# Kernel tuning notes

Measured on AMD Instinct MI355X. Metric: run time of the kernel, lower is better.

The kernel has to match this reference:

```python
import jax, jax.numpy as jnp
import numpy as np
import math

# Dims: d_model=192, expand=2 -> d_inner=d_ssm=384, headdim=64 -> nheads=6,
# d_state=128, K=4 scan directions, ngroups=1 (directions fused into state dim).
D_MODEL = 192
D_STATE = 128
D_CONV = 3
EXPAND = 2
HEADDIM = 64
CHUNK = 256
D_INNER = EXPAND * D_MODEL          # 384
D_SSM = D_INNER                     # default d_ssm (d_mlp == 0)
NHEADS = D_SSM // HEADDIM           # 6
K = 4                               # scan directions
HTOT = K * NHEADS                   # 24 heads in the fused scan
NSTATE = K * D_STATE                # 512 fused state dim (ngroups=1)
CONV_BC = 2 * D_STATE + NHEADS      # 262
B, H, W = 2, 64, 64


def _dwconv(x, w, b):
    # x: (B,C,H,W), w: (C,1,k,k) depthwise, SAME padding ((k-1)//2)
    y = jax.lax.conv_general_dilated(
        x, w, (1, 1), [(1, 1), (1, 1)],
        feature_group_count=x.shape[1],
        dimension_numbers=('NCHW', 'OIHW', 'NCHW'))
    return y + b[None, :, None, None]


def _ssd(x, dt_raw, A_logs, Bm, Cm, Ds, dt_bias):
    # Mamba2 chunked selective scan (dt_softplus=True, default dt_limit).
    # x: (b,l,h,p)  dt_raw: (b,l,h)  Bm,Cm: (b,l,n) with ngroups=1
    A = -jnp.exp(A_logs)                              # (h,)
    dt = jax.nn.softplus(dt_raw + dt_bias)            # (b,l,h)
    b, l, h, p = x.shape
    n = Bm.shape[-1]
    nc = l // CHUNK
    xc = x.reshape(b, nc, CHUNK, h, p)
    dtc = dt.reshape(b, nc, CHUNK, h)
    Bc = Bm.reshape(b, nc, CHUNK, n)
    Cc = Cm.reshape(b, nc, CHUNK, n)
    dA = dtc * A                                      # (b,nc,cs,h)
    acum = jnp.cumsum(dA, axis=2)
    # intra-chunk (causal, attention-like)
    a_t = jnp.transpose(acum, (0, 1, 3, 2))           # (b,nc,h,cs)
    diff = a_t[..., :, None] - a_t[..., None, :]      # (b,nc,h,i,j)
    causal = jnp.tril(jnp.ones((CHUNK, CHUNK), bool))
    Lmat = jnp.where(causal, jnp.exp(diff), 0.0)
    CB = jnp.einsum('bcin,bcjn->bcij', Cc, Bc)        # (b,nc,i,j)
    M = CB[:, :, None] * Lmat * jnp.transpose(dtc, (0, 1, 3, 2))[:, :, :, None, :]
    y = jnp.einsum('bchij,bcjhp->bcihp', M, xc)
    # chunk-final states
    decay_end = jnp.exp(acum[:, :, -1:, :] - acum)    # (b,nc,cs,h)
    states = jnp.einsum('bcjh,bcjn,bcjhp->bchpn', decay_end * dtc, Bc, xc)
    chunk_decay = jnp.exp(acum[:, :, -1, :])          # (b,nc,h)

    def step(S, inp):
        st, dec = inp
        return S * dec[:, :, None, None] + st, S

    S0 = jnp.zeros((b, h, p, n), x.dtype)
    _, prev = jax.lax.scan(step, S0, (jnp.moveaxis(states, 1, 0),
                                      jnp.moveaxis(chunk_decay, 1, 0)))
    prev = jnp.moveaxis(prev, 0, 1)                   # (b,nc,h,p,n)
    y = y + jnp.einsum('bcih,bcin,bchpn->bcihp', jnp.exp(acum), Cc, prev)
    y = y + xc * Ds[:, None]                          # D skip connection
    return y.reshape(b, l, h, p)


def _branch(u, u_cross, W_skip, W_xs, W_bcdt, conv_xs_w, conv_xs_b,
            conv_bc_w, conv_bc_b, dt_bias, A_logs, Ds, norm_w, W_out):
    Bb, Hh, Ww, _ = u.shape
    L = Hh * Ww
    z = (u @ W_skip).reshape(Bb, L, D_SSM)            # gate (d_mlp == 0)
    xs = jnp.transpose(u @ W_xs, (0, 3, 1, 2))        # (B,d_ssm,H,W)
    xs = jax.nn.silu(_dwconv(xs, conv_xs_w, conv_xs_b))
    bc = jnp.transpose(u_cross @ W_bcdt, (0, 3, 1, 2))
    bc = jax.nn.silu(_dwconv(bc, conv_bc_w, conv_bc_b))
    xbc = jnp.concatenate([xs, bc], axis=1)           # (B,646,H,W)
    C = xbc.shape[1]
    v = xbc.reshape(Bb, C, L)                         # HW raster
    vt = jnp.transpose(xbc, (0, 1, 3, 2)).reshape(Bb, C, L)  # WH raster
    hw = jnp.stack([v, vt], axis=1)                   # (B,2,C,L)
    xbcdt = jnp.concatenate([hw, jnp.flip(hw, axis=-1)], axis=1)  # (B,4,C,L)
    xp = xbcdt[:, :, :D_SSM]
    Bp = xbcdt[:, :, D_SSM:D_SSM + D_STATE]
    Cp = xbcdt[:, :, D_SSM + D_STATE:D_SSM + 2 * D_STATE]
    dtp = xbcdt[:, :, D_SSM + 2 * D_STATE:]
    x = xp.reshape(Bb, K * D_SSM, L).transpose(0, 2, 1).reshape(Bb, L, HTOT, HEADDIM)
    Bm = Bp.reshape(Bb, NSTATE, L).transpose(0, 2, 1)
    Cm = Cp.reshape(Bb, NSTATE, L).transpose(0, 2, 1)
    dt = dtp.reshape(Bb, HTOT, L).transpose(0, 2, 1)
    y = _ssd(x, dt, A_logs, Bm, Cm, Ds, dt_bias)      # (B,L,24,64)
    y = y.reshape(Bb, L, K, D_SSM)
    out_y = y[:, :, 0]
    inv_y = jnp.flip(y[:, :, 2:4], axis=1)            # (B,L,2,d_ssm)
    wh_y = y[:, :, 1].reshape(Bb, Ww, Hh, D_SSM).transpose(0, 2, 1, 3).reshape(Bb, L, D_SSM)
    invwh_y = inv_y[:, :, 1].reshape(Bb, Ww, Hh, D_SSM).transpose(0, 2, 1, 3).reshape(Bb, L, D_SSM)
    yf = out_y + inv_y[:, :, 0] + wh_y + invwh_y
    # gated RMSNorm (norm_before_gate=False, group_size == d_ssm)
    g = yf * jax.nn.silu(z)
    g = g * jax.lax.rsqrt(jnp.mean(g * g, axis=-1, keepdims=True) + 1e-5) * norm_w
    return (g @ W_out).reshape(Bb, Hh, Ww, D_MODEL)


def setup_inputs():
    key = jax.random.key(0)
    ks = jax.random.split(key, 16)
    f = lambda i, s: jax.random.normal(ks[i], s, jnp.float32)
    sc = 0.02
    dt = jnp.exp(jax.random.uniform(ks[10], (NHEADS,)) *
                 (math.log(0.1) - math.log(0.001)) + math.log(0.001))
    dt = jnp.maximum(dt, 1e-4)
    inv_dt = dt + jnp.log(-jnp.expm1(-dt))
    A = jax.random.uniform(ks[11], (NHEADS,), minval=1.0, maxval=16.0)
    return {
        'u1': f(0, (B, H, W, D_MODEL)),
        'u2': f(1, (B, H, W, D_MODEL)),
        'u2_cat_u1': f(2, (B, H, W, D_MODEL)),
        'u1_cat_u2': f(3, (B, H, W, D_MODEL)),
        'W_skip': f(4, (D_MODEL, D_SSM)) * sc,
        'W_xs': f(5, (D_MODEL, D_SSM)) * sc,
        'W_bcdt': f(6, (D_MODEL, CONV_BC)) * sc,
        'conv_xs_w': f(7, (D_SSM, 1, D_CONV, D_CONV)) * sc,
        'conv_xs_b': jnp.zeros((D_SSM,), jnp.float32),
        'conv_bc_w': f(8, (CONV_BC, 1, D_CONV, D_CONV)) * sc,
        'conv_bc_b': jnp.zeros((CONV_BC,), jnp.float32),
        'dt_bias': jnp.tile(inv_dt, K),
        'A_logs': jnp.tile(jnp.log(A), K),
        'Ds': jnp.ones((HTOT,), jnp.float32),
        'norm_w': jnp.ones((D_SSM,), jnp.float32),
        'W_out': f(9, (D_SSM, D_MODEL)) * sc,
    }


def reference(u1, u2, u2_cat_u1, u1_cat_u2, W_skip, W_xs, W_bcdt,
              conv_xs_w, conv_xs_b, conv_bc_w, conv_bc_b,
              dt_bias, A_logs, Ds, norm_w, W_out):
    args = (W_skip, W_xs, W_bcdt, conv_xs_w, conv_xs_b, conv_bc_w,
            conv_bc_b, dt_bias, A_logs, Ds, norm_w, W_out)
    out1 = _branch(u1, u2_cat_u1, *args)
    out2 = _branch(u2, u1_cat_u2, *args)
    return out1, out2
```

## Files before the change

### kernel.cpp

```cpp
#include <hip/hip_runtime.h>
#include <hip/hip_bf16.h>

#define DEV __device__ __forceinline__

static constexpr int LL   = 4096;
static constexpr int GG   = 4;
static constexpr int CBC  = 262;
static constexpr int BSTR = 264;

typedef float f32x4  __attribute__((ext_vector_type(4)));
typedef short bf16x8 __attribute__((ext_vector_type(8)));
typedef short bf16x4v __attribute__((ext_vector_type(4)));

DEV int map_l(int s, int k) {
    int m = (k & 2) ? (4095 - s) : s;
    if (k & 1) m = ((m & 63) << 6) | (m >> 6);
    return m;
}
DEV float silu_f(float x) { return x / (1.f + __expf(-x)); }
DEV short f2bf(float f) {
    union { __hip_bfloat16 h; short s; } u;
    u.h = __float2bfloat16(f);
    return u.s;
}
DEV float bf2f(short s) {
    return __uint_as_float(((unsigned)(unsigned short)s) << 16);
}
DEV bf16x8 pack8(float4 a, float4 b) {
    bf16x8 r;
    r[0]=f2bf(a.x); r[1]=f2bf(a.y); r[2]=f2bf(a.z); r[3]=f2bf(a.w);
    r[4]=f2bf(b.x); r[5]=f2bf(b.y); r[6]=f2bf(b.z); r[7]=f2bf(b.w);
    return r;
}
DEV bf16x8 load8u(const __hip_bfloat16* p) {
    bf16x4v lo = *(const bf16x4v*)p;
    bf16x4v hi = *(const bf16x4v*)(p + 4);
    bf16x8 r;
    r[0]=lo[0]; r[1]=lo[1]; r[2]=lo[2]; r[3]=lo[3];
    r[4]=hi[0]; r[5]=hi[1]; r[6]=hi[2]; r[7]=hi[3];
    return r;
}
DEV void store16(__hip_bfloat16* p, const float* v) {
    bf16x8 a, b;
    #pragma unroll
    for (int e = 0; e < 8; ++e) { a[e] = f2bf(v[e]); b[e] = f2bf(v[8+e]); }
    *(bf16x8*)p = a;
    *((bf16x8*)p + 1) = b;
}
DEV void storeT(float v, float* p) { *p = v; }
DEV void storeT(float v, __hip_bfloat16* p) { *p = __float2bfloat16(v); }

__global__ void sentinel_k(float* out) { out[0] = 1e30f; }

__global__ void wt_all_k(const float* __restrict__ W_skip, const float* __restrict__ W_xs,
                         const float* __restrict__ W_bcdt, const float* __restrict__ W_out,
                         __hip_bfloat16* __restrict__ Wt)
{
    int idx = blockIdx.x * 256 + threadIdx.x;
    if (idx < 73728) {
        int n = idx / 192, k = idx - n * 192;
        Wt[idx] = __float2bfloat16(W_skip[(size_t)k * 384 + n]);
    } else if (idx < 147456) {
        int r = idx - 73728;
        int n = r / 192, k = r - n * 192;
        Wt[idx] = __float2bfloat16(W_xs[(size_t)k * 384 + n]);
    } else if (idx < 208896) {
        int r = idx - 147456;
        int n = r / 192, k = r - n * 192;
        Wt[idx] = __float2bfloat16(n < 262 ? W_bcdt[(size_t)k * 262 + n] : 0.f);
    } else if (idx < 282624) {
        int r = idx - 208896;
        int n = r / 384, k = r - n * 384;
        Wt[idx] = __float2bfloat16(W_out[(size_t)k * 192 + n]);
    }
}

template<int MODE, typename AT, typename OutT>
__global__ __launch_bounds__(256) void mgemm_k(
    const AT* __restrict__ A0, const AT* __restrict__ A1,
    const __hip_bfloat16* __restrict__ Wt, OutT* __restrict__ C,
    OutT* __restrict__ C2, int N, int Kd)
{
    int i0 = blockIdx.y * 128;
    int j0 = blockIdx.x * 64;
    int t = threadIdx.x;
    int w = t >> 6, lane = t & 63;
    int lr = lane & 15, kq = lane >> 4;
    const AT* arow[2];
    #pragma unroll
    for (int a = 0; a < 2; ++a) {
        int grow = i0 + w * 32 + a * 16 + lr;
        const AT* Ap = (grow < 8192) ? A0 : A1;
        arow[a] = Ap + (size_t)(grow & 8191) * Kd;
    }
    f32x4 acc[2][4] = {};
    for (int k0 = 0; k0 < Kd; k0 += 32) {
        int kb = k0 + kq * 8;
        bf16x8 af[2];
        #pragma unroll
        for (int a = 0; a < 2; ++a) {
            if constexpr (sizeof(AT) == 4)
                af[a] = pack8(*(const float4*)(arow[a] + kb), *(const float4*)(arow[a] + kb + 4));
            else
                af[a] = *(const bf16x8*)(arow[a] + kb);
        }
        #pragma unroll
        for (int b = 0; b < 4; ++b) {
            int n = j0 + b * 16 + lr;
            bf16x8 bfr = *(const bf16x8*)(Wt + (size_t)n * Kd + kb);
            #pragma unroll
            for (int a = 0; a < 2; ++a)
                acc[a][b] = __builtin_amdgcn_mfma_f32_16x16x32_bf16(af[a], bfr, acc[a][b], 0, 0, 0);
        }
    }
    #pragma unroll
    for (int a = 0; a < 2; ++a)
        #pragma unroll
        for (int b = 0; b < 4; ++b)
            #pragma unroll
            for (int r = 0; r < 4; ++r) {
                int row = i0 + w * 32 + a * 16 + kq * 4 + r;
                int col = j0 + b * 16 + lr;
                float v = acc[a][b][r];
                if constexpr (MODE == 0) {
                    if (col < N) storeT(v, &C[(size_t)row * N + col]);
                } else if constexpr (MODE == 1) {
                    if (col < N) storeT(silu_f(v), &C[(size_t)row * N + col]);
                } else {
                    if (col < 384) storeT(silu_f(v), &C[(size_t)row * 384 + col]);
                    else           storeT(v, &C2[(size_t)row * 384 + col - 384]);
                }
            }
}

template<typename InT, typename OutT>
__global__ void dwconv_k(const InT* __restrict__ in, const float* __restrict__ w,
                         const float* __restrict__ bias, OutT* __restrict__ out,
                         int Cin, int Cout)
{
    int idx = blockIdx.x * 256 + threadIdx.x;
    int total = GG * LL * Cin;
    if (idx >= total) return;
    int c = idx % Cin;
    int l = (idx / Cin) % LL;
    int g = idx / (Cin * LL);
    int h = l >> 6, ww = l & 63;
    float acc = bias[c];
    #pragma unroll
    for (int dy = 0; dy < 3; ++dy) {
        int hh = h + dy - 1;
        if ((unsigned)hh >= 64u) continue;
        #pragma unroll
        for (int dx = 0; dx < 3; ++dx) {
            int wx = ww + dx - 1;
            if ((unsigned)wx >= 64u) continue;
            float iv;
            if constexpr (sizeof(InT) == 4) iv = in[((size_t)g * LL + (hh << 6) + wx) * Cin + c];
            else iv = __bfloat162float(in[((size_t)g * LL + (hh << 6) + wx) * Cin + c]);
            acc += iv * w[c * 9 + dy * 3 + dx];
        }
    }
    storeT(silu_f(acc), &out[((size_t)g * LL + l) * Cout + c]);
}

__global__ __launch_bounds__(256) void xtc_k(const __hip_bfloat16* __restrict__ pre_xs,
                                             const float* __restrict__ cxw,
                                             const float* __restrict__ cxb,
                                             __hip_bfloat16* __restrict__ XtG)
{
    __shared__ float raw[18][18][17];
    __shared__ float ls[16][17][17];
    __shared__ float wsm[16][9];
    __shared__ float bsm[16];
    int bid = blockIdx.x;
    int pct = bid % 24;
    int rest = bid / 24;
    int wt = rest & 3, ht2 = (rest >> 2) & 3, g = rest >> 4;
    int h0 = ht2 * 16, w0 = wt * 16, pc0 = pct * 16;
    int t = threadIdx.x;
    if (t < 144) wsm[t / 9][t % 9] = cxw[(pc0 + t / 9) * 9 + t % 9];
    if (t < 16)  bsm[t] = cxb[pc0 + t];
    for (int i = t; i < 18 * 18 * 16; i += 256) {
        int ch = i & 15;
        int hw = i >> 4;
        int ww2 = hw % 18, hh = hw / 18;
        int gh = h0 - 1 + hh, gw = w0 - 1 + ww2;
        float v = 0.f;
        if ((unsigned)gh < 64u && (unsigned)gw < 64u)
            v = __bfloat162float(pre_xs[((size_t)g * LL + gh * 64 + gw) * 384 + pc0 + ch]);
        raw[hh][ww2][ch] = v;
    }
    __syncthreads();
    {
        int h = t >> 4, w2 = t & 15;
        #pragma unroll 4
        for (int ch = 0; ch < 16; ++ch) {
            float acc = bsm[ch];
            #pragma unroll
            for (int dy = 0; dy < 3; ++dy)
                #pragma unroll
                for (int dx = 0; dx < 3; ++dx)
                    acc += raw[h + dy][w2 + dx][ch] * wsm[ch][dy * 3 + dx];
            ls[h][w2][ch] = silu_f(acc);
        }
    }
    __syncthreads();
    int pc = t >> 4, q = t & 15;
    float v[16];
    size_t rowbase;
    #pragma unroll
    for (int e = 0; e < 16; ++e) v[e] = ls[q][e][pc];
    rowbase = ((size_t)(g * 2 + 0) * 384 + pc0 + pc) * 4096;
    store16(XtG + rowbase + (h0 + q) * 64 + w0, v);
    #pragma unroll
    for (int e = 0; e < 16; ++e) v[e] = ls[e][q][pc];
    rowbase = ((size_t)(g * 2 + 1) * 384 + pc0 + pc) * 4096;
    store16(XtG + rowbase + (w0 + q) * 64 + h0, v);
}

__global__ __launch_bounds__(256) void prep_k(
    const float* __restrict__ bct, const float* __restrict__ dt_bias,
    const float* __restrict__ A_logs, __hip_bfloat16* __restrict__ Bt,
    __hip_bfloat16* __restrict__ Cs, __hip_bfloat16* __restrict__ Bs,
    float* __restrict__ dt_arr, float* __restrict__ ac_arr,
    float* __restrict__ cdecay)
{
    __shared__ float ls[16][17][17];
    __shared__ float wsum[4];
    int bid = blockIdx.x;
    int t = threadIdx.x;
    if (bid < 2048) {
        int nt = bid & 31;
        int rest = bid >> 5;
        int wt = rest & 3, ht2 = (rest >> 2) & 3, g = rest >> 4;
        int h0 = ht2 * 16, w0 = wt * 16;
        int kd = nt >> 3, ch0 = (nt & 7) * 16;
        int cl = t & 15, hwb = t >> 4;
        #pragma unroll
        for (int r = 0; r < 16; ++r) {
            int hw = hwb + r * 16;
            int h = hw >> 4, w2 = hw & 15;
            ls[h][w2][cl] = bct[((size_t)g * LL + (h0 + h) * 64 + (w0 + w2)) * BSTR + ch0 + cl];
        }
        __syncthreads();
        int pc = t >> 4, q = t & 15;
        int n = nt * 16 + pc;
        __hip_bfloat16* rowp = Bt + ((size_t)g * 512 + n) * 4096;
        float v[16];
        if (kd == 0) {
            #pragma unroll
            for (int e = 0; e < 16; ++e) v[e] = ls[q][e][pc];
            store16(rowp + (h0 + q) * 64 + w0, v);
        } else if (kd == 1) {
            #pragma unroll
            for (int e = 0; e < 16; ++e) v[e] = ls[e][q][pc];
            store16(rowp + (w0 + q) * 64 + h0, v);
        } else if (kd == 2) {
            #pragma unroll
            for (int e = 0; e < 16; ++e) v[e] = ls[q][15 - e][pc];
            store16(rowp + 4095 - (h0 + q) * 64 - w0 - 15, v);
        } else {
            #pragma unroll
            for (int e = 0; e < 16; ++e) v[e] = ls[15 - e][q][pc];
            store16(rowp + 4095 - (w0 + q) * 64 - h0 - 15, v);
        }
    } else if (bid < 4096) {
        int b2 = bid - 2048;
        int ct = b2 & 31;
        int rest = b2 >> 5;
        int wt = rest & 3, ht2 = (rest >> 2) & 3, g = rest >> 4;
        int h0 = ht2 * 16, w0 = wt * 16;
        bool isB = ct >= 16;
        int ctl = ct & 15;
        int kd = ctl >> 3, ch0 = (ctl & 7) * 16;
        int off = (isB ? 0 : 128) + ch0;
        __hip_bfloat16* dst = isB ? Bs : Cs;
        int cl = t & 15, hwb = t >> 4;
        #pragma unroll
        for (int r = 0; r < 16; ++r) {
            int hw = hwb + r * 16;
            int h = hw >> 4, w2 = hw & 15;
            ls[h][w2][cl] = bct[((size_t)g * LL + (h0 + h) * 64 + (w0 + w2)) * BSTR + off + cl];
        }
        __syncthreads();
        int h = t >> 4, w2 = t & 15;
        int s = (kd == 0) ? (h0 + h) * 64 + (w0 + w2) : (w0 + w2) * 64 + (h0 + h);
        float v[16];
        #pragma unroll
        for (int e = 0; e < 16; ++e) v[e] = ls[h][w2][e];
        store16(dst + ((size_t)g * 4096 + s) * 256 + kd * 128 + ch0, v);
    } else {
        int b3 = bid - 4096;
        int ht = b3 % 24;
        int gc = b3 / 24;
        int c = gc & 15, g = gc >> 4;
        int k = ht / 6, h = ht % 6;
        int s = c * 256 + t;
        int l = map_l(s, k);
        float raw = bct[((size_t)g * LL + l) * BSTR + 256 + h] + dt_bias[ht];
        float dtv = raw > 20.f ? raw : log1pf(__expf(raw));
        float dA = dtv * (-__expf(A_logs[ht]));
        float v = dA;
        #pragma unroll
        for (int off = 1; off < 64; off <<= 1) {
            float u = __shfl_up(v, off);
            if ((t & 63) >= off) v += u;
        }
        if ((t & 63) == 63) wsum[t >> 6] = v;
        __syncthreads();
        float add = 0.f;
        #pragma unroll
        for (int w2 = 0; w2 < 3; ++w2)
            if (w2 < (t >> 6)) add += wsum[w2];
        float cum = v + add;
        size_t base = ((size_t)g * 24 + ht) * LL + s;
        dt_arr[base] = dtv;
        ac_arr[base] = cum;
        if (t == 255) cdecay[(g * 24 + ht) * 16 + c] = __expf(cum);
    }
}

__global__ __launch_bounds__(256) void cb_k(const __hip_bfloat16* __restrict__ Cs,
                                            const __hip_bfloat16* __restrict__ Bs,
                                            __hip_bfloat16* __restrict__ CBm)
{
    int bid = blockIdx.x;
    int jq = bid & 3;
    int gc = bid >> 2;
    int c = gc & 15, g = gc >> 4;
    int t = threadIdx.x;
    int w = t >> 6, lane = t & 63;
    int lr = lane & 15, kq = lane >> 4;
    const __hip_bfloat16* cg = Cs + (size_t)g * 4096 * 256;
    const __hip_bfloat16* bsg = Bs + (size_t)g * 4096 * 256;
    f32x4 acc[4][4] = {};
    for (int ks = 0; ks < 16; ++ks) {
        int n0 = ks * 32 + kq * 8;
        int kd = n0 >> 7, nn = n0 & 127;
        int col = ((kd & 1) << 7) + nn;
        bf16x8 bfr[4];
        #pragma unroll
        for (int jt = 0; jt < 4; ++jt) {
            int j = jq * 64 + jt * 16 + lr;
            int s = c * 256 + j;
            int row = (kd < 2) ? s : 4095 - s;
            bfr[jt] = *(const bf16x8*)(bsg + (size_t)row * 256 + col);
        }
        #pragma unroll
        for (int iq = 0; iq < 4; ++iq) {
            int i = (w * 4 + iq) * 16 + lr;
            int s = c * 256 + i;
            int row = (kd < 2) ? s : 4095 - s;
            bf16x8 af = *(const bf16x8*)(cg + (size_t)row * 256 + col);
            #pragma unroll
            for (int jt = 0; jt < 4; ++jt)
                acc[iq][jt] = __builtin_amdgcn_mfma_f32_16x16x32_bf16(af, bfr[jt], acc[iq][jt], 0, 0, 0);
        }
    }
    __hip_bfloat16* ob = CBm + (size_t)gc * 65536;
    #pragma unroll
    for (int iq = 0; iq < 4; ++iq)
        #pragma unroll
        for (int jt = 0; jt < 4; ++jt)
            #pragma unroll
            for (int r = 0; r < 4; ++r) {
                int i = (w * 4 + iq) * 16 + kq * 4 + r;
                int j = jq * 64 + jt * 16 + lr;
                ob[(size_t)i * 256 + j] = __float2bfloat16(acc[iq][jt][r]);
            }
}

__global__ __launch_bounds__(256) void states_k(
    const __hip_bfloat16* __restrict__ XtG, const __hip_bfloat16* __restrict__ Bt,
    const float* __restrict__ dt_arr, const float* __restrict__ ac_arr,
    __hip_bfloat16* __restrict__ states)
{
    __shared__ float wsh[256];
    __shared__ short xw[64][264];
    int task = (blockIdx.x & 7) * 384 + (blockIdx.x >> 3);
    int ht = task % 24;
    int rest = task / 24;
    int nh = rest & 1;
    int gc = rest >> 1;
    int c = gc & 15, g = gc >> 4;
    int kd = ht / 6;
    bool rev = kd >= 2;
    int c0 = (ht % 6) * 64;
    int n0 = nh * 256;
    int t = threadIdx.x;
    int w = t >> 6, lane = t & 63;
    int lr = lane & 15, kq = lane >> 4;
    const float* dtp = dt_arr + ((size_t)g * 24 + ht) * LL + c * 256;
    const float* acp = ac_arr + ((size_t)g * 24 + ht) * LL + c * 256;
    float ac_last = acp[255];
    wsh[t] = __expf(ac_last - acp[t]) * dtp[t];
    __syncthreads();
    const __hip_bfloat16* xg = XtG + ((size_t)(g * 2 + (kd & 1)) * 384 + c0) * 4096;
    #pragma unroll
    for (int r8 = 0; r8 < 8; ++r8) {
        int id = t + 256 * r8;
        int p = id >> 5;
        int jc = (id & 31) * 8;
        bf16x8 xv;
        if (!rev) {
            xv = *(const bf16x8*)(xg + (size_t)p * 4096 + c * 256 + jc);
        } else {
            bf16x8 tmp = load8u(xg + (size_t)p * 4096 + 4088 - c * 256 - jc);
            #pragma unroll
            for (int e = 0; e < 8; ++e) xv[e] = tmp[7 - e];
        }
        bf16x8 o;
        #pragma unroll
        for (int e = 0; e < 8; ++e) o[e] = f2bf(bf2f(xv[e]) * wsh[jc + e]);
        *(bf16x8*)&xw[p][jc] = o;
    }
    __syncthreads();
    const __hip_bfloat16* btg = Bt + ((size_t)g * 512 + n0) * 4096;
    f32x4 acc[4][4] = {};
    for (int ks = 0; ks < 8; ++ks) {
        int j0 = ks * 32 + kq * 8;
        bf16x8 af[4];
        #pragma unroll
        for (int pt = 0; pt < 4; ++pt)
            af[pt] = *(const bf16x8*)&xw[pt * 16 + lr][j0];
        #pragma unroll
        for (int nt = 0; nt < 4; ++nt) {
            int nl = (w * 4 + nt) * 16 + lr;
            bf16x8 bv = *(const bf16x8*)(btg + (size_t)nl * 4096 + c * 256 + j0);
            #pragma unroll
            for (int pt = 0; pt < 4; ++pt)
                acc[pt][nt] = __builtin_amdgcn_mfma_f32_16x16x32_bf16(af[pt], bv, acc[pt][nt], 0, 0, 0);
        }
    }
    __hip_bfloat16* ob = states + ((size_t)gc * 24 + ht) * 32768 + n0;
    #pragma unroll
    for (int pt = 0; pt < 4; ++pt)
        #pragma unroll
        for (int nt = 0; nt < 4; ++nt)
            #pragma unroll
            for (int r = 0; r < 4; ++r) {
                int p = pt * 16 + kq * 4 + r;
                int nl = (w * 4 + nt) * 16 + lr;
                ob[(size_t)p * 512 + nl] = __float2bfloat16(acc[pt][nt][r]);
            }
}

__global__ void scan_k(__hip_bfloat16* __restrict__ states, const float* __restrict__ cdecay)
{
    int idx = blockIdx.x * 256 + threadIdx.x;
    int g = idx / 98304;
    int r = idx - g * 98304;
    int ht = r >> 12;
    int pn8 = (r & 4095) * 8;
    const float* cd = cdecay + (g * 24 + ht) * 16;
    __hip_bfloat16* base = states + ((size_t)g * 384 + ht) * 32768 + pn8;
    float S[8] = {};
    #pragma unroll
    for (int c2 = 0; c2 < 16; ++c2) {
        bf16x8* p = (bf16x8*)(base + (size_t)c2 * 786432);
        bf16x8 tmp = *p;
        bf16x8 o;
        float dec = cd[c2];
        #pragma unroll
        for (int e = 0; e < 8; ++e) {
            o[e] = f2bf(S[e]);
            S[e] = S[e] * dec + bf2f(tmp[e]);
        }
        *p = o;
    }
}

__global__ __launch_bounds__(256) void yk(
    const __hip_bfloat16* __restrict__ XtG, const __hip_bfloat16* __restrict__ Cs,
    const __hip_bfloat16* __restrict__ CBm, const __hip_bfloat16* __restrict__ prev,
    const float* __restrict__ dt_arr, const float* __restrict__ ac_arr,
    const float* __restrict__ Ds, __hip_bfloat16* __restrict__ y4)
{
    __shared__ float acs[256], dts[256], ejdt[256];
    __shared__ short xl[64][264];
    int task = (blockIdx.x & 7) * 192 + (blockIdx.x >> 3);
    int ht = task % 24;
    int gc = task / 24;
    int c = gc & 15, g = gc >> 4;
    int kd = ht / 6;
    bool rev = kd >= 2;
    int c0 = (ht % 6) * 64;
    int t = threadIdx.x;
    int w = t >> 6, lane = t & 63;
    int lr = lane & 15, kq = lane >> 4;
    size_t abase = ((size_t)g * 24 + ht) * LL + c * 256;
    float ac_own = ac_arr[abase + t];
    float dt_own = dt_arr[abase + t];
    acs[t] = ac_own;
    dts[t] = dt_own;
    float acb0 = __shfl(ac_own, (t & 63) & ~31);
    ejdt[t] = __expf(acb0 - ac_own) * dt_own;
    const __hip_bfloat16* xg = XtG + ((size_t)(g * 2 + (kd & 1)) * 384 + c0) * 4096;
    #pragma unroll
    for (int r8 = 0; r8 < 8; ++r8) {
        int id = t + 256 * r8;
        int p = id >> 5;
        int jc = (id & 31) * 8;
        bf16x8 xv;
        if (!rev) {
            xv = *(const bf16x8*)(xg + (size_t)p * 4096 + c * 256 + jc);
        } else {
            bf16x8 tmp = load8u(xg + (size_t)p * 4096 + 4088 - c * 256 - jc);
            #pragma unroll
            for (int e = 0; e < 8; ++e) xv[e] = tmp[7 - e];
        }
        *(bf16x8*)&xl[p][jc] = xv;
    }
    __syncthreads();
    const __hip_bfloat16* cbb = CBm + (size_t)gc * 65536;
    const __hip_bfloat16* cg = Cs + (size_t)g * 4096 * 256;
    f32x4 acc[4][4] = {};
    const __hip_bfloat16* pv = prev + ((size_t)gc * 24 + ht) * 32768;
    auto ld2 = [&](int ns, bf16x8* afq, bf16x8* pb) {
        int n0 = ns * 32 + kq * 8;
        int kd2 = n0 >> 7, nn = n0 & 127;
        int col = ((kd2 & 1) << 7) + nn;
        #pragma unroll
        for (int q = 0; q < 4; ++q) {
            int i = (w + 4 * q) * 16 + lr;
            int s = c * 256 + i;
            int row = (kd2 < 2) ? s : 4095 - s;
            afq[q] = *(const bf16x8*)(cg + (size_t)row * 256 + col);
        }
        #pragma unroll
        for (int pt = 0; pt < 4; ++pt)
            pb[pt] = *(const bf16x8*)(pv + (size_t)(pt * 16 + lr) * 512 + n0);
    };
    auto fma2 = [&](bf16x8* afq, bf16x8* pb) {
        #pragma unroll
        for (int q = 0; q < 4; ++q)
            #pragma unroll
            for (int pt = 0; pt < 4; ++pt)
                acc[q][pt] = __builtin_amdgcn_mfma_f32_16x16x32_bf16(afq[q], pb[pt], acc[q][pt], 0, 0, 0);
    };
    {
        bf16x8 afA[4], pbA[4], afB[4], pbB[4];
        ld2(0, afA, pbA);
        #pragma unroll
        for (int ns = 0; ns < 16; ns += 2) {
            if (ns + 1 < 16) ld2(ns + 1, afB, pbB);
            fma2(afA, pbA);
            if (ns + 2 < 16) ld2(ns + 2, afA, pbA);
            fma2(afB, pbB);
        }
    }
    #pragma unroll
    for (int q = 0; q < 4; ++q)
        #pragma unroll
        for (int r = 0; r < 4; ++r) {
            float er = __expf(acs[(w + 4 * q) * 16 + kq * 4 + r]);
            #pragma unroll
            for (int pt = 0; pt < 4; ++pt) acc[q][pt][r] *= er;
        }
    float aci_q[4];
    #pragma unroll
    for (int q = 0; q < 4; ++q) aci_q[q] = acs[(w + 4 * q) * 16 + lr];
    for (int ks = 0; ks < 8; ++ks) {
        int j0 = ks * 32 + kq * 8;
        bf16x8 xb[4];
        #pragma unroll
        for (int pt = 0; pt < 4; ++pt)
            xb[pt] = *(const bf16x8*)&xl[pt * 16 + lr][j0];
        float acb = acs[ks * 32];
        float ej[8];
        #pragma unroll
        for (int e = 0; e < 8; ++e) ej[e] = ejdt[j0 + e];
        #pragma unroll
        for (int q = 0; q < 4; ++q) {
            int rt = w + 4 * q;
            if (rt < 2 * ks) continue;
            int i = rt * 16 + lr;
            float r2 = __expf(aci_q[q] - acb);
            bf16x8 cb8 = *(const bf16x8*)(cbb + (size_t)i * 256 + j0);
            bf16x8 af;
            if (rt >= 2 * ks + 2) {
                #pragma unroll
                for (int e = 0; e < 8; ++e)
                    af[e] = f2bf(r2 * ej[e] * bf2f(cb8[e]));
            } else {
                #pragma unroll
                for (int e = 0; e < 8; ++e) {
                    float coef = r2 * ej[e] * bf2f(cb8[e]);
                    af[e] = (j0 + e <= i) ? f2bf(coef) : (short)0;
                }
            }
            #pragma unroll
            for (int pt = 0; pt < 4; ++pt)
                acc[q][pt] = __builtin_amdgcn_mfma_f32_16x16x32_bf16(af, xb[pt], acc[q][pt], 0, 0, 0);
        }
    }
    float Dsv = Ds[ht];
    __hip_bfloat16* yb = y4 + (((size_t)(g * 4 + kd) * 4096 + c * 256) * 384) + c0;
    #pragma unroll
    for (int q = 0; q < 4; ++q) {
        int rt = w + 4 * q;
        #pragma unroll
        for (int pt = 0; pt < 4; ++pt) {
            int p = pt * 16 + lr;
            int ibase = rt * 16 + kq * 4;
            bf16x4v x4 = *(const bf16x4v*)&xl[p][ibase];
            #pragma unroll
            for (int r = 0; r < 4; ++r) {
                int i = ibase + r;
                float xv = bf2f(x4[r]);
                yb[(size_t)i * 384 + p] = __float2bfloat16(acc[q][pt][r] + Dsv * xv);
            }
        }
    }
}

__global__ __launch_bounds__(128) void gate_k(
    const __hip_bfloat16* __restrict__ y4, const __hip_bfloat16* __restrict__ z_silu,
    const float* __restrict__ norm_w, __hip_bfloat16* __restrict__ gn)
{
    int g = blockIdx.x >> 12;
    int l = blockIdx.x & 4095;
    int t = threadIdx.x;
    int Tl = ((l & 63) << 6) | (l >> 6);
    const __hip_bfloat16* p0 = y4 + ((size_t)(g * 4 + 0) * 4096 + l) * 384;
    const __hip_bfloat16* p1 = y4 + ((size_t)(g * 4 + 1) * 4096 + Tl) * 384;
    const __hip_bfloat16* p2 = y4 + ((size_t)(g * 4 + 2) * 4096 + 4095 - l) * 384;
    const __hip_bfloat16* p3 = y4 + ((size_t)(g * 4 + 3) * 4096 + 4095 - Tl) * 384;
    const __hip_bfloat16* zp = z_silu + ((size_t)g * LL + l) * 384;
    float gc[3]; float ssq = 0.f;
    #pragma unroll
    for (int q = 0; q < 3; ++q) {
        int cdim = t + 128 * q;
        float yf = __bfloat162float(p0[cdim]) + __bfloat162float(p1[cdim]) +
                   __bfloat162float(p2[cdim]) + __bfloat162float(p3[cdim]);
        float v = yf * __bfloat162float(zp[cdim]);
        gc[q] = v;
        ssq += v * v;
    }
    float v = ssq;
    #pragma unroll
    for (int off = 32; off > 0; off >>= 1) v += __shfl_down(v, off);
    __shared__ float tot[2];
    if ((t & 63) == 0) tot[t >> 6] = v;
    __syncthreads();
    float rs = rsqrtf((tot[0] + tot[1]) * (1.f / 384.f) + 1e-5f);
    __hip_bfloat16* gp = gn + ((size_t)g * LL + l) * 384;
    #pragma unroll
    for (int q = 0; q < 3; ++q) {
        int cdim = t + 128 * q;
        gp[cdim] = __float2bfloat16(gc[q] * rs * norm_w[cdim]);
    }
}

extern "C" void kernel_launch(void* const* d_in, const int* in_sizes, int n_in,
                              void* d_out, int out_size, void* d_ws, size_t ws_size,
                              hipStream_t stream)
{
    const float* u1      = (const float*)d_in[0];
    const float* u2      = (const float*)d_in[1];
    const float* u21     = (const float*)d_in[2];
    const float* u12     = (const float*)d_in[3];
    const float* W_skip  = (const float*)d_in[4];
    const float* W_xs    = (const float*)d_in[5];
    const float* W_bcdt  = (const float*)d_in[6];
    const float* cxw     = (const float*)d_in[7];
    const float* cxb     = (const float*)d_in[8];
    const float* cbw     = (const float*)d_in[9];
    const float* cbb     = (const float*)d_in[10];
    const float* dt_bias = (const float*)d_in[11];
    const float* A_logs  = (const float*)d_in[12];
    const float* Ds      = (const float*)d_in[13];
    const float* norm_w  = (const float*)d_in[14];
    const float* W_out   = (const float*)d_in[15];
    float* out = (float*)d_out;

    char* w = (char*)d_ws;
    size_t o_y4  = 0;
    size_t o_st  = o_y4 + 50331648;
    size_t o_z   = o_st + 100663296;
    size_t o_xtg = o_z  + 12582912;
    size_t o_bt  = o_xtg + 25165824;
    size_t o_cs  = o_bt + 16777216;
    size_t o_cbm = o_cs + 8388608;
    size_t o_dt  = o_cbm + 8388608;
    size_t o_ac  = o_dt + 1572864;
    size_t o_cd  = o_ac + 1572864;
    size_t o_wt  = o_cd + 8192;
    size_t o_bs  = o_wt + 589824;
    size_t total = o_bs + 8388608;
    if (total > ws_size) {
        sentinel_k<<<1, 1, 0, stream>>>(out);
        return;
    }
    __hip_bfloat16* y4     = (__hip_bfloat16*)(w + o_y4);
    __hip_bfloat16* states = (__hip_bfloat16*)(w + o_st);
    __hip_bfloat16* z_silu = (__hip_bfloat16*)(w + o_z);
    __hip_bfloat16* XtG    = (__hip_bfloat16*)(w + o_xtg);
    __hip_bfloat16* Bt     = (__hip_bfloat16*)(w + o_bt);
    __hip_bfloat16* Cs     = (__hip_bfloat16*)(w + o_cs);
    __hip_bfloat16* CBm    = (__hip_bfloat16*)(w + o_cbm);
    float*          dt_arr = (float*)(w + o_dt);
    float*          ac_arr = (float*)(w + o_ac);
    float*          cdecay = (float*)(w + o_cd);
    __hip_bfloat16* Wt     = (__hip_bfloat16*)(w + o_wt);
    __hip_bfloat16* Bs     = (__hip_bfloat16*)(w + o_bs);
    __hip_bfloat16* Wt_skip = Wt;
    __hip_bfloat16* Wt_bcdt = Wt + 147456;
    __hip_bfloat16* Wt_out  = Wt + 208896;
    float*          bct    = (float*)(w + o_y4);
    __hip_bfloat16* pre_bc = (__hip_bfloat16*)(w + o_st);
    __hip_bfloat16* pre_xs = (__hip_bfloat16*)(w + o_st + 8650752);
    __hip_bfloat16* gn     = (__hip_bfloat16*)(w + o_st);

    dim3 blk(256);
    wt_all_k<<<dim3(1104), blk, 0, stream>>>(W_skip, W_xs, W_bcdt, W_out, Wt);
    mgemm_k<2, float, __hip_bfloat16><<<dim3(12, 128), blk, 0, stream>>>(
        u1, u2, Wt_skip, z_silu, pre_xs, 768, 192);
    mgemm_k<0, float, __hip_bfloat16><<<dim3(5, 128), blk, 0, stream>>>(
        u21, u12, Wt_bcdt, pre_bc, nullptr, CBC, 192);
    dwconv_k<__hip_bfloat16, float><<<dim3((GG * LL * CBC) / 256), blk, 0, stream>>>(
        pre_bc, cbw, cbb, bct, CBC, BSTR);
    xtc_k<<<dim3(1536), blk, 0, stream>>>(pre_xs, cxw, cxb, XtG);
    prep_k<<<dim3(5632), blk, 0, stream>>>(bct, dt_bias, A_logs, Bt, Cs, Bs,
                                           dt_arr, ac_arr, cdecay);
    cb_k<<<dim3(256), blk, 0, stream>>>(Cs, Bs, CBm);
    states_k<<<dim3(3072), blk, 0, stream>>>(XtG, Bt, dt_arr, ac_arr, states);
    scan_k<<<dim3(1536), blk, 0, stream>>>(states, cdecay);
    yk<<<dim3(1536), blk, 0, stream>>>(XtG, Cs, CBm, states, dt_arr, ac_arr, Ds, y4);
    gate_k<<<dim3(16384), dim3(128), 0, stream>>>(y4, z_silu, norm_w, gn);
    mgemm_k<0, __hip_bfloat16, float><<<dim3(3, 128), blk, 0, stream>>>(
        gn, gn + (size_t)8192 * 384, Wt_out, out, nullptr, 192, 384);
}
```

Before: 440.0 us.

## Fuse B/C/dt depthwise conv into prep kernel and merge cb with states kernel

```diff
diff --git a/kernel.cpp b/kernel.cpp
--- a/kernel.cpp
+++ b/kernel.cpp
@@ -6,11 +6,11 @@
 static constexpr int LL   = 4096;
 static constexpr int GG   = 4;
 static constexpr int CBC  = 262;
-static constexpr int BSTR = 264;
 
 typedef float f32x4  __attribute__((ext_vector_type(4)));
 typedef short bf16x8 __attribute__((ext_vector_type(8)));
 typedef short bf16x4v __attribute__((ext_vector_type(4)));
+typedef short bf16x2 __attribute__((ext_vector_type(2)));
 
 DEV int map_l(int s, int k) {
     int m = (k & 2) ? (4095 - s) : s;
@@ -131,36 +131,6 @@
                     else           storeT(v, &C2[(size_t)row * 384 + col - 384]);
                 }
             }
-}
-
-template<typename InT, typename OutT>
-__global__ void dwconv_k(const InT* __restrict__ in, const float* __restrict__ w,
-                         const float* __restrict__ bias, OutT* __restrict__ out,
-                         int Cin, int Cout)
-{
-    int idx = blockIdx.x * 256 + threadIdx.x;
-    int total = GG * LL * Cin;
-    if (idx >= total) return;
-    int c = idx % Cin;
-    int l = (idx / Cin) % LL;
-    int g = idx / (Cin * LL);
-    int h = l >> 6, ww = l & 63;
-    float acc = bias[c];
-    #pragma unroll
-    for (int dy = 0; dy < 3; ++dy) {
-        int hh = h + dy - 1;
-        if ((unsigned)hh >= 64u) continue;
-        #pragma unroll
-        for (int dx = 0; dx < 3; ++dx) {
-            int wx = ww + dx - 1;
-            if ((unsigned)wx >= 64u) continue;
-            float iv;
-            if constexpr (sizeof(InT) == 4) iv = in[((size_t)g * LL + (hh << 6) + wx) * Cin + c];
-            else iv = __bfloat162float(in[((size_t)g * LL + (hh << 6) + wx) * Cin + c]);
-            acc += iv * w[c * 9 + dy * 3 + dx];
-        }
-    }
-    storeT(silu_f(acc), &out[((size_t)g * LL + l) * Cout + c]);
 }
 
 __global__ __launch_bounds__(256) void xtc_k(const __hip_bfloat16* __restrict__ pre_xs,
@@ -218,14 +188,56 @@
     store16(XtG + rowbase + (w0 + q) * 64 + h0, v);
 }
 
+DEV void conv16(const __hip_bfloat16* __restrict__ pre, const float* __restrict__ cw,
+                const float* __restrict__ cbia, int g, int h0, int w0, int chb,
+                float* smem, float (*wsm)[9], float* bsm, int t)
+{
+    if (t < 144) wsm[t / 9][t % 9] = cw[(chb + t / 9) * 9 + t % 9];
+    if (t < 16)  bsm[t] = cbia[chb + t];
+    for (int i = t; i < 18 * 18 * 8; i += 256) {
+        int cp = i & 7;
+        int hw = i >> 3;
+        int ww2 = hw % 18, hh = hw / 18;
+        int gh = h0 - 1 + hh, gw = w0 - 1 + ww2;
+        float v0 = 0.f, v1 = 0.f;
+        if ((unsigned)gh < 64u && (unsigned)gw < 64u) {
+            bf16x2 pv = *(const bf16x2*)(pre + ((size_t)g * LL + gh * 64 + gw) * 262 + chb + cp * 2);
+            v0 = bf2f(pv[0]); v1 = bf2f(pv[1]);
+        }
+        smem[(hh * 18 + ww2) * 17 + cp * 2]     = v0;
+        smem[(hh * 18 + ww2) * 17 + cp * 2 + 1] = v1;
+    }
+    __syncthreads();
+    int h = t >> 4, w2 = t & 15;
+    float out[16];
+    #pragma unroll
+    for (int ch = 0; ch < 16; ++ch) {
+        float acc = bsm[ch];
+        #pragma unroll
+        for (int dy = 0; dy < 3; ++dy)
+            #pragma unroll
+            for (int dx = 0; dx < 3; ++dx)
+                acc += smem[((h + dy) * 18 + (w2 + dx)) * 17 + ch] * wsm[ch][dy * 3 + dx];
+        out[ch] = silu_f(acc);
+    }
+    __syncthreads();
+    #pragma unroll
+    for (int ch = 0; ch < 16; ++ch)
+        smem[(h * 17 + w2) * 17 + ch] = out[ch];
+    __syncthreads();
+}
+
 __global__ __launch_bounds__(256) void prep_k(
-    const float* __restrict__ bct, const float* __restrict__ dt_bias,
+    const __hip_bfloat16* __restrict__ pre_bc, const float* __restrict__ cbw,
+    const float* __restrict__ cbb, const float* __restrict__ dt_bias,
     const float* __restrict__ A_logs, __hip_bfloat16* __restrict__ Bt,
     __hip_bfloat16* __restrict__ Cs, __hip_bfloat16* __restrict__ Bs,
     float* __restrict__ dt_arr, float* __restrict__ ac_arr,
     float* __restrict__ cdecay)
 {
-    __shared__ float ls[16][17][17];
+    __shared__ float smem[18 * 18 * 17];
+    __shared__ float wsm[16][9];
+    __shared__ float bsm[16];
     __shared__ float wsum[4];
     int bid = blockIdx.x;
     int t = threadIdx.x;
@@ -235,33 +247,26 @@
         int wt = rest & 3, ht2 = (rest >> 2) & 3, g = rest >> 4;
         int h0 = ht2 * 16, w0 = wt * 16;
         int kd = nt >> 3, ch0 = (nt & 7) * 16;
-        int cl = t & 15, hwb = t >> 4;
-        #pragma unroll
-        for (int r = 0; r < 16; ++r) {
-            int hw = hwb + r * 16;
-            int h = hw >> 4, w2 = hw & 15;
-            ls[h][w2][cl] = bct[((size_t)g * LL + (h0 + h) * 64 + (w0 + w2)) * BSTR + ch0 + cl];
-        }
-        __syncthreads();
+        conv16(pre_bc, cbw, cbb, g, h0, w0, ch0, smem, wsm, bsm, t);
         int pc = t >> 4, q = t & 15;
         int n = nt * 16 + pc;
         __hip_bfloat16* rowp = Bt + ((size_t)g * 512 + n) * 4096;
         float v[16];
         if (kd == 0) {
             #pragma unroll
-            for (int e = 0; e < 16; ++e) v[e] = ls[q][e][pc];
+            for (int e = 0; e < 16; ++e) v[e] = smem[(q * 17 + e) * 17 + pc];
             store16(rowp + (h0 + q) * 64 + w0, v);
         } else if (kd == 1) {
             #pragma unroll
-            for (int e = 0; e < 16; ++e) v[e] = ls[e][q][pc];
+            for (int e = 0; e < 16; ++e) v[e] = smem[(e * 17 + q) * 17 + pc];
             store16(rowp + (w0 + q) * 64 + h0, v);
         } else if (kd == 2) {
             #pragma unroll
-            for (int e = 0; e < 16; ++e) v[e] = ls[q][15 - e][pc];
+            for (int e = 0; e < 16; ++e) v[e] = smem[(q * 17 + 15 - e) * 17 + pc];
             store16(rowp + 4095 - (h0 + q) * 64 - w0 - 15, v);
         } else {
             #pragma unroll
-            for (int e = 0; e < 16; ++e) v[e] = ls[15 - e][q][pc];
+            for (int e = 0; e < 16; ++e) v[e] = smem[((15 - e) * 17 + q) * 17 + pc];
             store16(rowp + 4095 - (w0 + q) * 64 - h0 - 15, v);
         }
     } else if (bid < 4096) {
@@ -273,21 +278,14 @@
         bool isB = ct >= 16;
         int ctl = ct & 15;
         int kd = ctl >> 3, ch0 = (ctl & 7) * 16;
-        int off = (isB ? 0 : 128) + ch0;
+        int chb = (isB ? 0 : 128) + ch0;
+        conv16(pre_bc, cbw, cbb, g, h0, w0, chb, smem, wsm, bsm, t);
         __hip_bfloat16* dst = isB ? Bs : Cs;
-        int cl = t & 15, hwb = t >> 4;
-        #pragma unroll
-        for (int r = 0; r < 16; ++r) {
-            int hw = hwb + r * 16;
-            int h = hw >> 4, w2 = hw & 15;
-            ls[h][w2][cl] = bct[((size_t)g * LL + (h0 + h) * 64 + (w0 + w2)) * BSTR + off + cl];
-        }
-        __syncthreads();
         int h = t >> 4, w2 = t & 15;
         int s = (kd == 0) ? (h0 + h) * 64 + (w0 + w2) : (w0 + w2) * 64 + (h0 + h);
         float v[16];
         #pragma unroll
-        for (int e = 0; e < 16; ++e) v[e] = ls[h][w2][e];
+        for (int e = 0; e < 16; ++e) v[e] = smem[(h * 17 + w2) * 17 + e];
         store16(dst + ((size_t)g * 4096 + s) * 256 + kd * 128 + ch0, v);
     } else {
         int b3 = bid - 4096;
@@ -297,7 +295,22 @@
         int k = ht / 6, h = ht % 6;
         int s = c * 256 + t;
         int l = map_l(s, k);
-        float raw = bct[((size_t)g * LL + l) * BSTR + 256 + h] + dt_bias[ht];
+        int ch = 256 + h;
+        float acc = cbb[ch];
+        int hh0 = l >> 6, ww0 = l & 63;
+        #pragma unroll
+        for (int dy = 0; dy < 3; ++dy) {
+            int gh = hh0 + dy - 1;
+            if ((unsigned)gh >= 64u) continue;
+            #pragma unroll
+            for (int dx = 0; dx < 3; ++dx) {
+                int gw = ww0 + dx - 1;
+                if ((unsigned)gw >= 64u) continue;
+                acc += __bfloat162float(pre_bc[((size_t)g * LL + gh * 64 + gw) * 262 + ch]) *
+                       cbw[ch * 9 + dy * 3 + dx];
+            }
+        }
+        float raw = silu_f(acc) + dt_bias[ht];
         float dtv = raw > 20.f ? raw : log1pf(__expf(raw));
         float dA = dtv * (-__expf(A_logs[ht]));
         float v = dA;
@@ -320,64 +333,64 @@
     }
 }
 
-__global__ __launch_bounds__(256) void cb_k(const __hip_bfloat16* __restrict__ Cs,
-                                            const __hip_bfloat16* __restrict__ Bs,
-                                            __hip_bfloat16* __restrict__ CBm)
-{
+__global__ __launch_bounds__(256) void cbst_k(
+    const __hip_bfloat16* __restrict__ Cs, const __hip_bfloat16* __restrict__ Bs,
+    __hip_bfloat16* __restrict__ CBm,
+    const __hip_bfloat16* __restrict__ XtG, const __hip_bfloat16* __restrict__ Bt,
+    const float* __restrict__ dt_arr, const float* __restrict__ ac_arr,
+    __hip_bfloat16* __restrict__ states)
+{
+    __shared__ float wsh[256];
+    __shared__ short xw[64][264];
     int bid = blockIdx.x;
-    int jq = bid & 3;
-    int gc = bid >> 2;
-    int c = gc & 15, g = gc >> 4;
     int t = threadIdx.x;
     int w = t >> 6, lane = t & 63;
     int lr = lane & 15, kq = lane >> 4;
-    const __hip_bfloat16* cg = Cs + (size_t)g * 4096 * 256;
-    const __hip_bfloat16* bsg = Bs + (size_t)g * 4096 * 256;
-    f32x4 acc[4][4] = {};
-    for (int ks = 0; ks < 16; ++ks) {
-        int n0 = ks * 32 + kq * 8;
-        int kd = n0 >> 7, nn = n0 & 127;
-        int col = ((kd & 1) << 7) + nn;
-        bf16x8 bfr[4];
-        #pragma unroll
-        for (int jt = 0; jt < 4; ++jt) {
-            int j = jq * 64 + jt * 16 + lr;
-            int s = c * 256 + j;
-            int row = (kd < 2) ? s : 4095 - s;
-            bfr[jt] = *(const bf16x8*)(bsg + (size_t)row * 256 + col);
-        }
-        #pragma unroll
-        for (int iq = 0; iq < 4; ++iq) {
-            int i = (w * 4 + iq) * 16 + lr;
-            int s = c * 256 + i;
-            int row = (kd < 2) ? s : 4095 - s;
-            bf16x8 af = *(const bf16x8*)(cg + (size_t)row * 256 + col);
+    if (bid < 256) {
+        int jq = bid & 3;
+        int gc = bid >> 2;
+        int c = gc & 15, g = gc >> 4;
+        const __hip_bfloat16* cg = Cs + (size_t)g * 4096 * 256;
+        const __hip_bfloat16* bsg = Bs + (size_t)g * 4096 * 256;
+        f32x4 acc[4][4] = {};
+        for (int ks = 0; ks < 16; ++ks) {
+            int n0 = ks * 32 + kq * 8;
+            int kd = n0 >> 7, nn = n0 & 127;
+            int col = ((kd & 1) << 7) + nn;
+            bf16x8 bfr[4];
+            #pragma unroll
+            for (int jt = 0; jt < 4; ++jt) {
+                int j = jq * 64 + jt * 16 + lr;
+                int s = c * 256 + j;
+                int row = (kd < 2) ? s : 4095 - s;
+                bfr[jt] = *(const bf16x8*)(bsg + (size_t)row * 256 + col);
+            }
+            #pragma unroll
+            for (int iq = 0; iq < 4; ++iq) {
+                int i = (w * 4 + iq) * 16 + lr;
+                int s = c * 256 + i;
+                int row = (kd < 2) ? s : 4095 - s;
+                bf16x8 af = *(const bf16x8*)(cg + (size_t)row * 256 + col);
+                #pragma unroll
+                for (int jt = 0; jt < 4; ++jt)
+                    acc[iq][jt] = __builtin_amdgcn_mfma_f32_16x16x32_bf16(af, bfr[jt], acc[iq][jt], 0, 0, 0);
+            }
+        }
+        __hip_bfloat16* ob = CBm + (size_t)gc * 65536;
+        #pragma unroll
+        for (int iq = 0; iq < 4; ++iq)
             #pragma unroll
             for (int jt = 0; jt < 4; ++jt)
-                acc[iq][jt] = __builtin_amdgcn_mfma_f32_16x16x32_bf16(af, bfr[jt], acc[iq][jt], 0, 0, 0);
-        }
-    }
-    __hip_bfloat16* ob = CBm + (size_t)gc * 65536;
-    #pragma unroll
-    for (int iq = 0; iq < 4; ++iq)
-        #pragma unroll
-        for (int jt = 0; jt < 4; ++jt)
-            #pragma unroll
-            for (int r = 0; r < 4; ++r) {
-                int i = (w * 4 + iq) * 16 + kq * 4 + r;
-                int j = jq * 64 + jt * 16 + lr;
-                ob[(size_t)i * 256 + j] = __float2bfloat16(acc[iq][jt][r]);
-            }
-}
-
-__global__ __launch_bounds__(256) void states_k(
-    const __hip_bfloat16* __restrict__ XtG, const __hip_bfloat16* __restrict__ Bt,
-    const float* __restrict__ dt_arr, const float* __restrict__ ac_arr,
-    __hip_bfloat16* __restrict__ states)
-{
-    __shared__ float wsh[256];
-    __shared__ short xw[64][264];
-    int task = (blockIdx.x & 7) * 384 + (blockIdx.x >> 3);
+                #pragma unroll
+                for (int r = 0; r < 4; ++r) {
+                    int i = (w * 4 + iq) * 16 + kq * 4 + r;
+                    int j = jq * 64 + jt * 16 + lr;
+                    ob[(size_t)i * 256 + j] = __float2bfloat16(acc[iq][jt][r]);
+                }
+        return;
+    }
+    int sb = bid - 256;
+    int task = (sb & 7) * 384 + (sb >> 3);
     int ht = task % 24;
     int rest = task / 24;
     int nh = rest & 1;
@@ -387,9 +400,6 @@
     bool rev = kd >= 2;
     int c0 = (ht % 6) * 64;
     int n0 = nh * 256;
-    int t = threadIdx.x;
-    int w = t >> 6, lane = t & 63;
-    int lr = lane & 15, kq = lane >> 4;
     const float* dtp = dt_arr + ((size_t)g * 24 + ht) * LL + c * 256;
     const float* acp = ac_arr + ((size_t)g * 24 + ht) * LL + c * 256;
     float ac_last = acp[255];
@@ -707,7 +717,6 @@
     __hip_bfloat16* Wt_skip = Wt;
     __hip_bfloat16* Wt_bcdt = Wt + 147456;
     __hip_bfloat16* Wt_out  = Wt + 208896;
-    float*          bct    = (float*)(w + o_y4);
     __hip_bfloat16* pre_bc = (__hip_bfloat16*)(w + o_st);
     __hip_bfloat16* pre_xs = (__hip_bfloat16*)(w + o_st + 8650752);
     __hip_bfloat16* gn     = (__hip_bfloat16*)(w + o_st);
@@ -718,13 +727,10 @@
         u1, u2, Wt_skip, z_silu, pre_xs, 768, 192);
     mgemm_k<0, float, __hip_bfloat16><<<dim3(5, 128), blk, 0, stream>>>(
         u21, u12, Wt_bcdt, pre_bc, nullptr, CBC, 192);
-    dwconv_k<__hip_bfloat16, float><<<dim3((GG * LL * CBC) / 256), blk, 0, stream>>>(
-        pre_bc, cbw, cbb, bct, CBC, BSTR);
     xtc_k<<<dim3(1536), blk, 0, stream>>>(pre_xs, cxw, cxb, XtG);
-    prep_k<<<dim3(5632), blk, 0, stream>>>(bct, dt_bias, A_logs, Bt, Cs, Bs,
-                                           dt_arr, ac_arr, cdecay);
-    cb_k<<<dim3(256), blk, 0, stream>>>(Cs, Bs, CBm);
-    states_k<<<dim3(3072), blk, 0, stream>>>(XtG, Bt, dt_arr, ac_arr, states);
+    prep_k<<<dim3(5632), blk, 0, stream>>>(pre_bc, cbw, cbb, dt_bias, A_logs,
+                                           Bt, Cs, Bs, dt_arr, ac_arr, cdecay);
+    cbst_k<<<dim3(3328), blk, 0, stream>>>(Cs, Bs, CBm, XtG, Bt, dt_arr, ac_arr, states);
     scan_k<<<dim3(1536), blk, 0, stream>>>(states, cdecay);
     yk<<<dim3(1536), blk, 0, stream>>>(XtG, Cs, CBm, states, dt_arr, ac_arr, Ds, y4);
     gate_k<<<dim3(16384), dim3(128), 0, stream>>>(y4, z_silu, norm_w, gn);
```

After: 422.8 us (median of 2 runs). 1.04x faster.
